# Kernel optimization log

Hardware: AMD Instinct MI355X
Metric: run time of the kernel (lower is better)

The kernel has to match this reference:

```python
import math
import jax, jax.numpy as jnp
import numpy as np

N_EXPERTS = 8
N_ACTIVE = 5
N_CAMP_A = 4
TEMPERATURE = math.e


def setup_inputs() -> dict:
    key = jax.random.key(0)
    ks = jax.random.split(key, 5)
    B, T, D, I = 4, 2048, 2048, 1024
    s = 0.02
    return {
        "x": jax.random.normal(ks[0], (B, T, D), jnp.float32),
        "Wr": jax.random.normal(ks[1], (D, N_EXPERTS), jnp.float32) * s,
        "Wg": jax.random.normal(ks[2], (N_EXPERTS, D, I), jnp.float32) * s,
        "Wu": jax.random.normal(ks[3], (N_EXPERTS, D, I), jnp.float32) * s,
        "Wd": jax.random.normal(ks[4], (N_EXPERTS, I, D), jnp.float32) * s,
    }


def _router_weights(x, Wr):
    # scores: (B,T,E)
    probs = jax.nn.softmax(jnp.einsum("btd,de->bte", x, Wr) / TEMPERATURE, axis=-1)
    _, topk_idx = jax.lax.top_k(probs, N_ACTIVE)          # (B,T,k)
    mask = jax.nn.one_hot(topk_idx, N_EXPERTS, dtype=probs.dtype).sum(axis=-2)
    w = probs * mask
    return w / (w.sum(axis=-1, keepdims=True) + 1e-8)


def reference(x, Wr, Wg, Wu, Wd):
    weights = _router_weights(x, Wr)                       # (B,T,E)
    # All experts run on full dense input (faithful to source loop), batched GEMMs.
    g = jnp.einsum("btd,edi->btei", x, Wg)                 # (B,T,E,I)
    u = jnp.einsum("btd,edi->btei", x, Wu)
    h = jax.nn.silu(g) * u
    eo = jnp.einsum("btei,eid->bted", h, Wd)               # (B,T,E,D)
    sign = jnp.concatenate([jnp.ones(N_CAMP_A), -jnp.ones(N_EXPERTS - N_CAMP_A)]).astype(x.dtype)
    output = jnp.einsum("bte,bted->btd", weights * sign, eo)  # out_a - out_g
    tension_scalar = jax.lax.stop_gradient(jnp.mean(output ** 2))
    return output, tension_scalar
```

## Files before the change

kernel.cpp:

```cpp
#include <hip/hip_runtime.h>
#include <cstdint>
#include <cstddef>


typedef short bf16x8 __attribute__((ext_vector_type(8)));
typedef float f32x4 __attribute__((ext_vector_type(4)));
typedef unsigned short u16;

typedef const unsigned int __attribute__((address_space(1)))* as1_u32p;
typedef unsigned int __attribute__((address_space(3)))* as3_u32p;

#define VMCNT6 asm volatile("s_waitcnt vmcnt(6)" ::: "memory")
#define VMCNT0 asm volatile("s_waitcnt vmcnt(0)" ::: "memory")
#define LGKM0  asm volatile("s_waitcnt lgkmcnt(0)" ::: "memory")
#define SBAR   __builtin_amdgcn_s_barrier()
#define SCHED0 __builtin_amdgcn_sched_barrier(0)
#define MFMA16(af, bf, cf) __builtin_amdgcn_mfma_f32_16x16x32_bf16(af, bf, cf, 0, 0, 0)

__device__ __forceinline__ u16 f2bf(float f) {
  unsigned u = __builtin_bit_cast(unsigned, f);
  u += 0x7fffu + ((u >> 16) & 1u);
  return (u16)(u >> 16);
}

__device__ __forceinline__ void gload16(const void* g, const u16* lds) {
  as1_u32p gp = (as1_u32p)(uintptr_t)g;
  as3_u32p lp = (as3_u32p)(unsigned)(uintptr_t)lds;
  __builtin_amdgcn_global_load_lds(gp, lp, 16, 0, 0);
}

__global__ __launch_bounds__(256) void router_kernel(
    const float* __restrict__ x, const float* __restrict__ Wr,
    float* __restrict__ Cw, u16* __restrict__ Xb) {
  const int l = threadIdx.x & 63;
  const int t = blockIdx.x * 4 + (threadIdx.x >> 6);
  const float* xr = x + (size_t)t * 2048;
  u16* xbr = Xb + (size_t)t * 2048;
  float p[8] = {0.f,0.f,0.f,0.f,0.f,0.f,0.f,0.f};
#pragma unroll
  for (int it = 0; it < 8; ++it) {
    const int d0 = it * 256 + l * 4;
    const float4 xv = *(const float4*)(xr + d0);
    unsigned lo = (unsigned)f2bf(xv.x) | ((unsigned)f2bf(xv.y) << 16);
    unsigned hi = (unsigned)f2bf(xv.z) | ((unsigned)f2bf(xv.w) << 16);
    *(unsigned*)(xbr + d0) = lo;
    *(unsigned*)(xbr + d0 + 2) = hi;
    const float xs[4] = {xv.x, xv.y, xv.z, xv.w};
#pragma unroll
    for (int jj = 0; jj < 4; ++jj) {
      const float4 w0 = *(const float4*)(Wr + (size_t)(d0 + jj) * 8);
      const float4 w1 = *(const float4*)(Wr + (size_t)(d0 + jj) * 8 + 4);
      p[0] += xs[jj] * w0.x; p[1] += xs[jj] * w0.y;
      p[2] += xs[jj] * w0.z; p[3] += xs[jj] * w0.w;
      p[4] += xs[jj] * w1.x; p[5] += xs[jj] * w1.y;
      p[6] += xs[jj] * w1.z; p[7] += xs[jj] * w1.w;
    }
  }
#pragma unroll
  for (int e = 0; e < 8; ++e) {
    float v = p[e];
#pragma unroll
    for (int off = 32; off > 0; off >>= 1) v += __shfl_xor(v, off, 64);
    p[e] = v;
  }
  constexpr float INV_TEMP = 0.36787944117144233f;
  float mx = -1e30f;
#pragma unroll
  for (int e = 0; e < 8; ++e) { p[e] *= INV_TEMP; mx = fmaxf(mx, p[e]); }
  float sum = 0.f;
#pragma unroll
  for (int e = 0; e < 8; ++e) { p[e] = __expf(p[e] - mx); sum += p[e]; }
  const float inv_sum = 1.f / sum;
#pragma unroll
  for (int e = 0; e < 8; ++e) p[e] *= inv_sum;
  unsigned sel = 0xFFu;
  for (int it = 0; it < 3; ++it) {
    float mn = 1e30f; int mi = 0;
#pragma unroll
    for (int e = 0; e < 8; ++e)
      if ((sel >> e) & 1u) { if (p[e] <= mn) { mn = p[e]; mi = e; } }
    sel &= ~(1u << mi);
  }
  float wsum = 0.f;
#pragma unroll
  for (int e = 0; e < 8; ++e) if ((sel >> e) & 1u) wsum += p[e];
  const float inv_w = 1.f / (wsum + 1e-8f);
  if (l == 0) {
#pragma unroll
    for (int e = 0; e < 8; ++e) {
      float v = ((sel >> e) & 1u) ? p[e] * inv_w : 0.f;
      Cw[(size_t)t * 8 + e] = (e < 4) ? v : -v;
    }
  }
}

__global__ __launch_bounds__(256) void tcvt_kernel(
    const float* __restrict__ in, u16* __restrict__ out,
    int R, int C, long long ZO, long long CS) {
  __shared__ float tile[32][33];
  const int z = blockIdx.z;
  const float* ib = in + (size_t)z * R * C;
  const int r0 = blockIdx.y * 32, c0 = blockIdx.x * 32;
  const int tx = threadIdx.x, ty = threadIdx.y;
#pragma unroll
  for (int j = 0; j < 4; ++j)
    tile[ty + j * 8][tx] = ib[(size_t)(r0 + ty + j * 8) * C + c0 + tx];
  __syncthreads();
#pragma unroll
  for (int j = 0; j < 4; ++j)
    out[(size_t)z * ZO + (size_t)(c0 + ty + j * 8) * CS + r0 + tx] =
        f2bf(tile[tx][ty + j * 8]);
}


__global__ __launch_bounds__(512, 2) void gemm1_8p(
    const u16* __restrict__ Xb, const u16* __restrict__ Wgt,
    const u16* __restrict__ Wut, const float* __restrict__ Cw,
    u16* __restrict__ Hp, int p) {
  extern __shared__ u16 lds[];
  const int tid = threadIdx.x;
  const int l = tid & 63, w = tid >> 6;
  const int wr = w >> 2, wc = w & 3;
  const int lq = l >> 4, lr = l & 15;
  const int bid = blockIdx.x;
  const int work = (bid & 7) * 128 + (bid >> 3);
  const int mtile = work & 31;
  const int en = work >> 5;
  const int el = en >> 3, nt = en & 7;
  const int e = p * 4 + el;
  const u16* gA  = Xb + (size_t)mtile * 256 * 2048;
  const u16* s0p = Wgt + (size_t)e * 2097152 + (size_t)nt * 128 * 2048;
  const u16* s1p = Wut + (size_t)e * 2097152 + (size_t)nt * 128 * 2048;
  const u16* s2p = gA;
  const u16* s3p = gA + (size_t)128 * 2048;
  const int NT = 32;

  auto stageU = [&](int tt, const u16* srcb, int u) {
    if (tt >= NT) return;
    u16* dst = lds + (tt & 1) * 32768 + u * 8192;
    const int kt = tt * 64;
#pragma unroll
    for (int j = 0; j < 2; ++j) {
      const int g = j * 512 + tid;
      const int row = g >> 3;
      const int cg = (g & 7) ^ (row & 7);
      gload16(srcb + (size_t)row * 2048 + kt + cg * 8, dst + g * 8);
    }
  };

  const int xr = lr & 7;
  const int x0 = (lq ^ xr) * 8;
  const int x1 = ((4 + lq) ^ xr) * 8;
  const int aB = (2 + wr) * 8192 + lr * 64;
  const int gBo = (wc * 32 + lr) * 64;
  const int uBo = 8192 + (wc * 32 + lr) * 64;

  bf16x8 a[8][2], bg[2][2], bu[2][2];
  f32x4 ag[8][2], au[8][2];
#pragma unroll
  for (int mi = 0; mi < 8; ++mi)
#pragma unroll
    for (int ni = 0; ni < 2; ++ni) {
      ag[mi][ni] = (f32x4){0.f, 0.f, 0.f, 0.f};
      au[mi][ni] = (f32x4){0.f, 0.f, 0.f, 0.f};
    }

  stageU(0, s0p, 0); stageU(0, s1p, 1); stageU(0, s2p, 2); stageU(0, s3p, 3);
  stageU(1, s0p, 0); stageU(1, s1p, 1); stageU(1, s2p, 2);
  VMCNT6; SBAR;

  for (int t = 0; t < NT; ++t) {
    const u16* Lb = lds + (t & 1) * 32768;
    {
#pragma unroll
      for (int mi = 0; mi < 4; ++mi) {
        a[mi][0] = *(const bf16x8*)&Lb[aB + mi * 1024 + x0];
        a[mi][1] = *(const bf16x8*)&Lb[aB + mi * 1024 + x1];
      }
#pragma unroll
      for (int ni = 0; ni < 2; ++ni) {
        bg[ni][0] = *(const bf16x8*)&Lb[gBo + ni * 1024 + x0];
        bg[ni][1] = *(const bf16x8*)&Lb[gBo + ni * 1024 + x1];
      }
      stageU(t + 1, s3p, 3);
      SBAR; LGKM0; SCHED0;
      __builtin_amdgcn_s_setprio(1);
#pragma unroll
      for (int mi = 0; mi < 4; ++mi)
#pragma unroll
        for (int ni = 0; ni < 2; ++ni)
#pragma unroll
          for (int kk = 0; kk < 2; ++kk)
            ag[mi][ni] = MFMA16(a[mi][kk], bg[ni][kk], ag[mi][ni]);
      __builtin_amdgcn_s_setprio(0); SCHED0; SBAR;
    }
    {
#pragma unroll
      for (int ni = 0; ni < 2; ++ni) {
        bu[ni][0] = *(const bf16x8*)&Lb[uBo + ni * 1024 + x0];
        bu[ni][1] = *(const bf16x8*)&Lb[uBo + ni * 1024 + x1];
      }
      stageU(t + 2, s0p, 0);
      SBAR; LGKM0; SCHED0;
      __builtin_amdgcn_s_setprio(1);
#pragma unroll
      for (int mi = 0; mi < 4; ++mi)
#pragma unroll
        for (int ni = 0; ni < 2; ++ni)
#pragma unroll
          for (int kk = 0; kk < 2; ++kk)
            au[mi][ni] = MFMA16(a[mi][kk], bu[ni][kk], au[mi][ni]);
      __builtin_amdgcn_s_setprio(0); SCHED0; SBAR;
    }
    {
#pragma unroll
      for (int mi = 4; mi < 8; ++mi) {
        a[mi][0] = *(const bf16x8*)&Lb[aB + mi * 1024 + x0];
        a[mi][1] = *(const bf16x8*)&Lb[aB + mi * 1024 + x1];
      }
      stageU(t + 2, s1p, 1);
      SBAR; LGKM0; SCHED0;
      __builtin_amdgcn_s_setprio(1);
#pragma unroll
      for (int mi = 4; mi < 8; ++mi)
#pragma unroll
        for (int ni = 0; ni < 2; ++ni)
#pragma unroll
          for (int kk = 0; kk < 2; ++kk)
            ag[mi][ni] = MFMA16(a[mi][kk], bg[ni][kk], ag[mi][ni]);
      __builtin_amdgcn_s_setprio(0); SCHED0; SBAR;
    }
    {
      stageU(t + 2, s2p, 2);
      if (t < NT - 2) { VMCNT6; } else if (t == NT - 2) { VMCNT0; }
      SBAR; LGKM0; SCHED0;
      __builtin_amdgcn_s_setprio(1);
#pragma unroll
      for (int mi = 4; mi < 8; ++mi)
#pragma unroll
        for (int ni = 0; ni < 2; ++ni)
#pragma unroll
          for (int kk = 0; kk < 2; ++kk)
            au[mi][ni] = MFMA16(a[mi][kk], bu[ni][kk], au[mi][ni]);
      __builtin_amdgcn_s_setprio(0); SCHED0; SBAR;
    }
  }

  __syncthreads();
  float* cl = (float*)lds;
  if (tid < 256) cl[tid] = Cw[(size_t)(mtile * 256 + tid) * 8 + e];
  __syncthreads();
#pragma unroll
  for (int mi = 0; mi < 8; ++mi) {
#pragma unroll
    for (int j = 0; j < 4; ++j) {
      const int rl = wr * 128 + mi * 16 + lq * 4 + j;
      const float c = cl[rl];
      const size_t row = (size_t)mtile * 256 + rl;
#pragma unroll
      for (int ni = 0; ni < 2; ++ni) {
        const float g = ag[mi][ni][j], u = au[mi][ni][j];
        const float h = g * (1.f / (1.f + __expf(-g))) * u * c;
        Hp[row * 4096 + el * 1024 + nt * 128 + wc * 32 + ni * 16 + lr] = f2bf(h);
      }
    }
  }
}

__global__ __launch_bounds__(512, 2) void gemm2_8p(
    const u16* __restrict__ Hp, const u16* __restrict__ Wdt,
    float* __restrict__ out, int koff, int accum) {
  extern __shared__ u16 lds[];
  const int tid = threadIdx.x;
  const int l = tid & 63, w = tid >> 6;
  const int wr = w >> 2, wc = w & 3;
  const int lq = l >> 4, lr = l & 15;
  const int bid = blockIdx.x;
  const int work = (bid & 7) * 32 + (bid >> 3);
  const int mtile = work & 31, ntile = work >> 5;
  const u16* gA = Hp + (size_t)mtile * 256 * 4096;
  const u16* gB = Wdt + (size_t)ntile * 256 * 8192 + koff;
  const u16* s0p = gB;
  const u16* s1p = gB + (size_t)128 * 8192;
  const u16* s2p = gA;
  const u16* s3p = gA + (size_t)128 * 4096;
  const int NT = 64;

  auto stageU = [&](int tt, const u16* srcb, int stride, int u) {
    if (tt >= NT) return;
    u16* dst = lds + (tt & 1) * 32768 + u * 8192;
    const int kt = tt * 64;
#pragma unroll
    for (int j = 0; j < 2; ++j) {
      const int g = j * 512 + tid;
      const int row = g >> 3;
      const int cg = (g & 7) ^ (row & 7);
      gload16(srcb + (size_t)row * stride + kt + cg * 8, dst + g * 8);
    }
  };

  const int xr = lr & 7;
  const int x0 = (lq ^ xr) * 8;
  const int x1 = ((4 + lq) ^ xr) * 8;
  const int aB = (2 + wr) * 8192 + lr * 64;
  const int bB = (wc >> 1) * 8192 + ((wc & 1) * 64 + lr) * 64;

  bf16x8 a[8][2], b[4][2];
  f32x4 acc[8][4];
#pragma unroll
  for (int mi = 0; mi < 8; ++mi)
#pragma unroll
    for (int ni = 0; ni < 4; ++ni) acc[mi][ni] = (f32x4){0.f, 0.f, 0.f, 0.f};

  stageU(0, s0p, 8192, 0); stageU(0, s1p, 8192, 1);
  stageU(0, s2p, 4096, 2); stageU(0, s3p, 4096, 3);
  stageU(1, s0p, 8192, 0); stageU(1, s1p, 8192, 1); stageU(1, s2p, 4096, 2);
  VMCNT6; SBAR;

  for (int t = 0; t < NT; ++t) {
    const u16* Lb = lds + (t & 1) * 32768;
    {
#pragma unroll
      for (int mi = 0; mi < 4; ++mi) {
        a[mi][0] = *(const bf16x8*)&Lb[aB + mi * 1024 + x0];
        a[mi][1] = *(const bf16x8*)&Lb[aB + mi * 1024 + x1];
      }
#pragma unroll
      for (int ni = 0; ni < 2; ++ni) {
        b[ni][0] = *(const bf16x8*)&Lb[bB + ni * 1024 + x0];
        b[ni][1] = *(const bf16x8*)&Lb[bB + ni * 1024 + x1];
      }
      if (wc < 2) {
#pragma unroll
        for (int ni = 2; ni < 4; ++ni) {
          b[ni][0] = *(const bf16x8*)&Lb[bB + ni * 1024 + x0];
          b[ni][1] = *(const bf16x8*)&Lb[bB + ni * 1024 + x1];
        }
      }
      stageU(t + 1, s3p, 4096, 3);
      SBAR; LGKM0; SCHED0;
      __builtin_amdgcn_s_setprio(1);
#pragma unroll
      for (int mi = 0; mi < 4; ++mi)
#pragma unroll
        for (int ni = 0; ni < 2; ++ni)
#pragma unroll
          for (int kk = 0; kk < 2; ++kk)
            acc[mi][ni] = MFMA16(a[mi][kk], b[ni][kk], acc[mi][ni]);
      __builtin_amdgcn_s_setprio(0); SCHED0; SBAR;
    }
    {
      if (wc >= 2) {
#pragma unroll
        for (int ni = 2; ni < 4; ++ni) {
          b[ni][0] = *(const bf16x8*)&Lb[bB + ni * 1024 + x0];
          b[ni][1] = *(const bf16x8*)&Lb[bB + ni * 1024 + x1];
        }
      }
      stageU(t + 2, s0p, 8192, 0);
      SBAR; LGKM0; SCHED0;
      __builtin_amdgcn_s_setprio(1);
#pragma unroll
      for (int mi = 0; mi < 4; ++mi)
#pragma unroll
        for (int ni = 2; ni < 4; ++ni)
#pragma unroll
          for (int kk = 0; kk < 2; ++kk)
            acc[mi][ni] = MFMA16(a[mi][kk], b[ni][kk], acc[mi][ni]);
      __builtin_amdgcn_s_setprio(0); SCHED0; SBAR;
    }
    {
#pragma unroll
      for (int mi = 4; mi < 8; ++mi) {
        a[mi][0] = *(const bf16x8*)&Lb[aB + mi * 1024 + x0];
        a[mi][1] = *(const bf16x8*)&Lb[aB + mi * 1024 + x1];
      }
      stageU(t + 2, s1p, 8192, 1);
      SBAR; LGKM0; SCHED0;
      __builtin_amdgcn_s_setprio(1);
#pragma unroll
      for (int mi = 4; mi < 8; ++mi)
#pragma unroll
        for (int ni = 2; ni < 4; ++ni)
#pragma unroll
          for (int kk = 0; kk < 2; ++kk)
            acc[mi][ni] = MFMA16(a[mi][kk], b[ni][kk], acc[mi][ni]);
      __builtin_amdgcn_s_setprio(0); SCHED0; SBAR;
    }
    {
      stageU(t + 2, s2p, 4096, 2);
      if (t < NT - 2) { VMCNT6; } else if (t == NT - 2) { VMCNT0; }
      SBAR; LGKM0; SCHED0;
      __builtin_amdgcn_s_setprio(1);
#pragma unroll
      for (int mi = 4; mi < 8; ++mi)
#pragma unroll
        for (int ni = 0; ni < 2; ++ni)
#pragma unroll
          for (int kk = 0; kk < 2; ++kk)
            acc[mi][ni] = MFMA16(a[mi][kk], b[ni][kk], acc[mi][ni]);
      __builtin_amdgcn_s_setprio(0); SCHED0; SBAR;
    }
  }

#pragma unroll
  for (int mi = 0; mi < 8; ++mi)
#pragma unroll
    for (int ni = 0; ni < 4; ++ni)
#pragma unroll
      for (int j = 0; j < 4; ++j) {
        const int row = mtile * 256 + wr * 128 + mi * 16 + lq * 4 + j;
        const int col = ntile * 256 + wc * 64 + ni * 16 + lr;
        const size_t idx = (size_t)row * 2048 + col;
        float v = acc[mi][ni][j];
        if (accum) v += out[idx];
        out[idx] = v;
      }
}

__global__ __launch_bounds__(256) void sqsum_partial(
    const float* __restrict__ out, float* __restrict__ part, int n4) {
  float s = 0.f;
  const int idx = blockIdx.x * 256 + threadIdx.x;
  const int stride = gridDim.x * 256;
  for (int i = idx; i < n4; i += stride) {
    const float4 v = ((const float4*)out)[i];
    s += v.x * v.x + v.y * v.y + v.z * v.z + v.w * v.w;
  }
#pragma unroll
  for (int off = 32; off > 0; off >>= 1) s += __shfl_down(s, off, 64);
  __shared__ float ls[4];
  if ((threadIdx.x & 63) == 0) ls[threadIdx.x >> 6] = s;
  __syncthreads();
  if (threadIdx.x == 0) part[blockIdx.x] = ls[0] + ls[1] + ls[2] + ls[3];
}

__global__ __launch_bounds__(256) void sqsum_final(
    const float* __restrict__ part, float* __restrict__ dst, int np, float scale) {
  float s = 0.f;
  for (int i = threadIdx.x; i < np; i += 256) s += part[i];
#pragma unroll
  for (int off = 32; off > 0; off >>= 1) s += __shfl_down(s, off, 64);
  __shared__ float ls[4];
  if ((threadIdx.x & 63) == 0) ls[threadIdx.x >> 6] = s;
  __syncthreads();
  if (threadIdx.x == 0) dst[0] = (ls[0] + ls[1] + ls[2] + ls[3]) * scale;
}

extern "C" void kernel_launch(void* const* d_in, const int* in_sizes, int n_in,
                              void* d_out, int out_size, void* d_ws, size_t ws_size,
                              hipStream_t stream) {
  (void)in_sizes; (void)n_in; (void)out_size; (void)ws_size;
  const float* x  = (const float*)d_in[0];
  const float* Wr = (const float*)d_in[1];
  const float* Wg = (const float*)d_in[2];
  const float* Wu = (const float*)d_in[3];
  const float* Wd = (const float*)d_in[4];
  float* out = (float*)d_out;
  char* ws = (char*)d_ws;
  u16*   Xb   = (u16*)(ws);
  u16*   Wgt  = (u16*)(ws + 33554432);
  u16*   Wut  = (u16*)(ws + 67108864);
  u16*   Wdt  = (u16*)(ws + 100663296);
  u16*   Hp   = (u16*)(ws + 134217728);
  float* Cw   = (float*)(ws + 201326592);
  float* part = (float*)(ws + 201588736);

  (void)hipFuncSetAttribute((const void*)gemm1_8p,
                            hipFuncAttributeMaxDynamicSharedMemorySize, 131072);
  (void)hipFuncSetAttribute((const void*)gemm2_8p,
                            hipFuncAttributeMaxDynamicSharedMemorySize, 131072);

  router_kernel<<<2048, 256, 0, stream>>>(x, Wr, Cw, Xb);

  dim3 tb(32, 8);
  tcvt_kernel<<<dim3(32, 64, 8), tb, 0, stream>>>(Wg, Wgt, 2048, 1024, 2097152LL, 2048LL);
  tcvt_kernel<<<dim3(32, 64, 8), tb, 0, stream>>>(Wu, Wut, 2048, 1024, 2097152LL, 2048LL);
  tcvt_kernel<<<dim3(64, 32, 8), tb, 0, stream>>>(Wd, Wdt, 1024, 2048, 1024LL, 8192LL);

  for (int p = 0; p < 2; ++p) {
    gemm1_8p<<<1024, 512, 131072, stream>>>(Xb, Wgt, Wut, Cw, Hp, p);
    gemm2_8p<<<256, 512, 131072, stream>>>(Hp, Wdt, out, p * 4096, p);
  }

  sqsum_partial<<<1024, 256, 0, stream>>>(out, part, 16777216 / 4);
  sqsum_final<<<1, 256, 0, stream>>>(part, out + 16777216, 1024, 1.f / 16777216.f);
}
```

Measured before the change: 884.6 us.

## Make gemm1 persistent over four N-tiles per block and transpose router weights

gemm1 now launches 256 blocks instead of 1024. Each block loops over four (expert, N-tile) work items while keeping the same X row tile, and the weight-tile prefetch runs continuously across item boundaries. The epilogue reads the combine weights from a transposed expert-major array with float4 loads, which removes the LDS staging and syncthreads. Load addressing is precomputed and an extra partial lgkmcnt wait is added before the barrier. The intent is to cut launch and tail overhead and pipeline bubbles between tiles, at the cost of fewer, longer blocks that may balance worse across CUs.

```diff
diff --git a/kernel.cpp b/kernel.cpp
--- a/kernel.cpp
+++ b/kernel.cpp
@@ -13,6 +13,7 @@
 #define VMCNT6 asm volatile("s_waitcnt vmcnt(6)" ::: "memory")
 #define VMCNT0 asm volatile("s_waitcnt vmcnt(0)" ::: "memory")
 #define LGKM0  asm volatile("s_waitcnt lgkmcnt(0)" ::: "memory")
+#define LGKM8  asm volatile("s_waitcnt lgkmcnt(8)" ::: "memory")
 #define SBAR   __builtin_amdgcn_s_barrier()
 #define SCHED0 __builtin_amdgcn_sched_barrier(0)
 #define MFMA16(af, bf, cf) __builtin_amdgcn_mfma_f32_16x16x32_bf16(af, bf, cf, 0, 0, 0)
@@ -31,7 +32,7 @@
 
 __global__ __launch_bounds__(256) void router_kernel(
     const float* __restrict__ x, const float* __restrict__ Wr,
-    float* __restrict__ Cw, u16* __restrict__ Xb) {
+    float* __restrict__ CwT, u16* __restrict__ Xb) {
   const int l = threadIdx.x & 63;
   const int t = blockIdx.x * 4 + (threadIdx.x >> 6);
   const float* xr = x + (size_t)t * 2048;
@@ -89,7 +90,7 @@
 #pragma unroll
     for (int e = 0; e < 8; ++e) {
       float v = ((sel >> e) & 1u) ? p[e] * inv_w : 0.f;
-      Cw[(size_t)t * 8 + e] = (e < 4) ? v : -v;
+      CwT[(size_t)e * 8192 + t] = (e < 4) ? v : -v;
     }
   }
 }
@@ -115,37 +116,40 @@
 
 __global__ __launch_bounds__(512, 2) void gemm1_8p(
     const u16* __restrict__ Xb, const u16* __restrict__ Wgt,
-    const u16* __restrict__ Wut, const float* __restrict__ Cw,
+    const u16* __restrict__ Wut, const float* __restrict__ CwT,
     u16* __restrict__ Hp, int p) {
   extern __shared__ u16 lds[];
   const int tid = threadIdx.x;
   const int l = tid & 63, w = tid >> 6;
   const int wr = w >> 2, wc = w & 3;
   const int lq = l >> 4, lr = l & 15;
-  const int bid = blockIdx.x;
-  const int work = (bid & 7) * 128 + (bid >> 3);
-  const int mtile = work & 31;
-  const int en = work >> 5;
-  const int el = en >> 3, nt = en & 7;
-  const int e = p * 4 + el;
+  const int b = blockIdx.x;
+  const int xcd = b & 7;
+  const int mtile = b >> 3;
+  const int en0 = xcd * 4;
   const u16* gA  = Xb + (size_t)mtile * 256 * 2048;
-  const u16* s0p = Wgt + (size_t)e * 2097152 + (size_t)nt * 128 * 2048;
-  const u16* s1p = Wut + (size_t)e * 2097152 + (size_t)nt * 128 * 2048;
   const u16* s2p = gA;
   const u16* s3p = gA + (size_t)128 * 2048;
-  const int NT = 32;
-
-  auto stageU = [&](int tt, const u16* srcb, int u) {
-    if (tt >= NT) return;
-    u16* dst = lds + (tt & 1) * 32768 + u * 8192;
-    const int kt = tt * 64;
-#pragma unroll
-    for (int j = 0; j < 2; ++j) {
-      const int g = j * 512 + tid;
-      const int row = g >> 3;
-      const int cg = (g & 7) ^ (row & 7);
-      gload16(srcb + (size_t)row * 2048 + kt + cg * 8, dst + g * 8);
-    }
+
+  const int row0 = tid >> 3,          cg0 = (tid & 7) ^ (row0 & 7);
+  const int row1 = (512 + tid) >> 3,  cg1 = ((512 + tid) & 7) ^ (row1 & 7);
+  const int off0 = row0 * 2048 + cg0 * 8;
+  const int off1 = row1 * 2048 + cg1 * 8;
+  const int d0e = tid * 8, d1e = (512 + tid) * 8;
+
+  auto bptr = [&](const u16* base, int item) -> const u16* {
+    const int it = item > 3 ? 3 : item;
+    const int en = en0 + it;
+    return base + (size_t)(p * 4 + (en >> 3)) * 2097152 +
+           (size_t)(en & 7) * 128 * 2048;
+  };
+
+  auto stageV = [&](int vt2, const u16* srcb, int u) {
+    if (vt2 >= 128) return;
+    u16* dst = lds + (vt2 & 1) * 32768 + u * 8192;
+    const int kt = (vt2 & 31) * 64;
+    gload16(srcb + (size_t)(off0 + kt), dst + d0e);
+    gload16(srcb + (size_t)(off1 + kt), dst + d1e);
   };
 
   const int xr = lr & 7;
@@ -165,12 +169,18 @@
       au[mi][ni] = (f32x4){0.f, 0.f, 0.f, 0.f};
     }
 
-  stageU(0, s0p, 0); stageU(0, s1p, 1); stageU(0, s2p, 2); stageU(0, s3p, 3);
-  stageU(1, s0p, 0); stageU(1, s1p, 1); stageU(1, s2p, 2);
+  const u16* bgS = bptr(Wgt, 0);
+  const u16* buS = bptr(Wut, 0);
+  int item_c = 0;
+
+  stageV(0, bgS, 0); stageV(0, buS, 1); stageV(0, s2p, 2); stageV(0, s3p, 3);
+  stageV(1, bgS, 0); stageV(1, buS, 1); stageV(1, s2p, 2);
   VMCNT6; SBAR;
 
-  for (int t = 0; t < NT; ++t) {
-    const u16* Lb = lds + (t & 1) * 32768;
+  for (int vt = 0; vt < 128; ++vt) {
+    const int t = vt & 31;
+    if (t == 30) { bgS = bptr(Wgt, item_c + 1); buS = bptr(Wut, item_c + 1); }
+    const u16* Lb = lds + (vt & 1) * 32768;
     {
 #pragma unroll
       for (int mi = 0; mi < 4; ++mi) {
@@ -182,8 +192,8 @@
         bg[ni][0] = *(const bf16x8*)&Lb[gBo + ni * 1024 + x0];
         bg[ni][1] = *(const bf16x8*)&Lb[gBo + ni * 1024 + x1];
       }
-      stageU(t + 1, s3p, 3);
-      SBAR; LGKM0; SCHED0;
+      stageV(vt + 1, s3p, 3);
+      LGKM8; SBAR; LGKM0; SCHED0;
       __builtin_amdgcn_s_setprio(1);
 #pragma unroll
       for (int mi = 0; mi < 4; ++mi)
@@ -200,7 +210,7 @@
         bu[ni][0] = *(const bf16x8*)&Lb[uBo + ni * 1024 + x0];
         bu[ni][1] = *(const bf16x8*)&Lb[uBo + ni * 1024 + x1];
       }
-      stageU(t + 2, s0p, 0);
+      stageV(vt + 2, bgS, 0);
       SBAR; LGKM0; SCHED0;
       __builtin_amdgcn_s_setprio(1);
 #pragma unroll
@@ -218,7 +228,7 @@
         a[mi][0] = *(const bf16x8*)&Lb[aB + mi * 1024 + x0];
         a[mi][1] = *(const bf16x8*)&Lb[aB + mi * 1024 + x1];
       }
-      stageU(t + 2, s1p, 1);
+      stageV(vt + 2, buS, 1);
       SBAR; LGKM0; SCHED0;
       __builtin_amdgcn_s_setprio(1);
 #pragma unroll
@@ -231,8 +241,8 @@
       __builtin_amdgcn_s_setprio(0); SCHED0; SBAR;
     }
     {
-      stageU(t + 2, s2p, 2);
-      if (t < NT - 2) { VMCNT6; } else if (t == NT - 2) { VMCNT0; }
+      stageV(vt + 2, s2p, 2);
+      if (vt < 126) { VMCNT6; } else if (vt == 126) { VMCNT0; }
       SBAR; LGKM0; SCHED0;
       __builtin_amdgcn_s_setprio(1);
 #pragma unroll
@@ -244,25 +254,35 @@
             au[mi][ni] = MFMA16(a[mi][kk], bu[ni][kk], au[mi][ni]);
       __builtin_amdgcn_s_setprio(0); SCHED0; SBAR;
     }
-  }
-
-  __syncthreads();
-  float* cl = (float*)lds;
-  if (tid < 256) cl[tid] = Cw[(size_t)(mtile * 256 + tid) * 8 + e];
-  __syncthreads();
-#pragma unroll
-  for (int mi = 0; mi < 8; ++mi) {
-#pragma unroll
-    for (int j = 0; j < 4; ++j) {
-      const int rl = wr * 128 + mi * 16 + lq * 4 + j;
-      const float c = cl[rl];
-      const size_t row = (size_t)mtile * 256 + rl;
-#pragma unroll
-      for (int ni = 0; ni < 2; ++ni) {
-        const float g = ag[mi][ni][j], u = au[mi][ni][j];
-        const float h = g * (1.f / (1.f + __expf(-g))) * u * c;
-        Hp[row * 4096 + el * 1024 + nt * 128 + wc * 32 + ni * 16 + lr] = f2bf(h);
-      }
+    if (t == 31) {
+      const int en = en0 + item_c;
+      const int el = en >> 3, nt = en & 7, e = p * 4 + el;
+      const float* cb = CwT + (size_t)e * 8192 + mtile * 256;
+#pragma unroll
+      for (int mi = 0; mi < 8; ++mi) {
+        const int r0 = wr * 128 + mi * 16 + lq * 4;
+        const float4 c4 = *(const float4*)(cb + r0);
+        const float cs[4] = {c4.x, c4.y, c4.z, c4.w};
+#pragma unroll
+        for (int j = 0; j < 4; ++j) {
+          const size_t row = (size_t)mtile * 256 + r0 + j;
+#pragma unroll
+          for (int ni = 0; ni < 2; ++ni) {
+            const float g = ag[mi][ni][j], u = au[mi][ni][j];
+            const float h = g * (1.f / (1.f + __expf(-g))) * u * cs[j];
+            Hp[row * 4096 + el * 1024 + nt * 128 + wc * 32 + ni * 16 + lr] =
+                f2bf(h);
+          }
+        }
+      }
+      ++item_c;
+#pragma unroll
+      for (int mi = 0; mi < 8; ++mi)
+#pragma unroll
+        for (int ni = 0; ni < 2; ++ni) {
+          ag[mi][ni] = (f32x4){0.f, 0.f, 0.f, 0.f};
+          au[mi][ni] = (f32x4){0.f, 0.f, 0.f, 0.f};
+        }
     }
   }
 }
@@ -286,17 +306,25 @@
   const u16* s3p = gA + (size_t)128 * 4096;
   const int NT = 64;
 
-  auto stageU = [&](int tt, const u16* srcb, int stride, int u) {
+  const int row0 = tid >> 3,          cg0 = (tid & 7) ^ (row0 & 7);
+  const int row1 = (512 + tid) >> 3,  cg1 = ((512 + tid) & 7) ^ (row1 & 7);
+  const int offA0 = row0 * 4096 + cg0 * 8, offA1 = row1 * 4096 + cg1 * 8;
+  const int offB0 = row0 * 8192 + cg0 * 8, offB1 = row1 * 8192 + cg1 * 8;
+  const int d0e = tid * 8, d1e = (512 + tid) * 8;
+
+  auto stageA = [&](int tt, const u16* srcb, int u) {
     if (tt >= NT) return;
     u16* dst = lds + (tt & 1) * 32768 + u * 8192;
     const int kt = tt * 64;
-#pragma unroll
-    for (int j = 0; j < 2; ++j) {
-      const int g = j * 512 + tid;
-      const int row = g >> 3;
-      const int cg = (g & 7) ^ (row & 7);
-      gload16(srcb + (size_t)row * stride + kt + cg * 8, dst + g * 8);
-    }
+    gload16(srcb + (size_t)(offA0 + kt), dst + d0e);
+    gload16(srcb + (size_t)(offA1 + kt), dst + d1e);
+  };
+  auto stageB = [&](int tt, const u16* srcb, int u) {
+    if (tt >= NT) return;
+    u16* dst = lds + (tt & 1) * 32768 + u * 8192;
+    const int kt = tt * 64;
+    gload16(srcb + (size_t)(offB0 + kt), dst + d0e);
+    gload16(srcb + (size_t)(offB1 + kt), dst + d1e);
   };
 
   const int xr = lr & 7;
@@ -312,9 +340,8 @@
 #pragma unroll
     for (int ni = 0; ni < 4; ++ni) acc[mi][ni] = (f32x4){0.f, 0.f, 0.f, 0.f};
 
-  stageU(0, s0p, 8192, 0); stageU(0, s1p, 8192, 1);
-  stageU(0, s2p, 4096, 2); stageU(0, s3p, 4096, 3);
-  stageU(1, s0p, 8192, 0); stageU(1, s1p, 8192, 1); stageU(1, s2p, 4096, 2);
+  stageB(0, s0p, 0); stageB(0, s1p, 1); stageA(0, s2p, 2); stageA(0, s3p, 3);
+  stageB(1, s0p, 0); stageB(1, s1p, 1); stageA(1, s2p, 2);
   VMCNT6; SBAR;
 
   for (int t = 0; t < NT; ++t) {
@@ -337,8 +364,8 @@
           b[ni][1] = *(const bf16x8*)&Lb[bB + ni * 1024 + x1];
         }
       }
-      stageU(t + 1, s3p, 4096, 3);
-      SBAR; LGKM0; SCHED0;
+      stageA(t + 1, s3p, 3);
+      LGKM8; SBAR; LGKM0; SCHED0;
       __builtin_amdgcn_s_setprio(1);
 #pragma unroll
       for (int mi = 0; mi < 4; ++mi)
@@ -357,7 +384,7 @@
           b[ni][1] = *(const bf16x8*)&Lb[bB + ni * 1024 + x1];
         }
       }
-      stageU(t + 2, s0p, 8192, 0);
+      stageB(t + 2, s0p, 0);
       SBAR; LGKM0; SCHED0;
       __builtin_amdgcn_s_setprio(1);
 #pragma unroll
@@ -375,7 +402,7 @@
         a[mi][0] = *(const bf16x8*)&Lb[aB + mi * 1024 + x0];
         a[mi][1] = *(const bf16x8*)&Lb[aB + mi * 1024 + x1];
       }
-      stageU(t + 2, s1p, 8192, 1);
+      stageB(t + 2, s1p, 1);
       SBAR; LGKM0; SCHED0;
       __builtin_amdgcn_s_setprio(1);
 #pragma unroll
@@ -388,7 +415,7 @@
       __builtin_amdgcn_s_setprio(0); SCHED0; SBAR;
     }
     {
-      stageU(t + 2, s2p, 4096, 2);
+      stageA(t + 2, s2p, 2);
       if (t < NT - 2) { VMCNT6; } else if (t == NT - 2) { VMCNT0; }
       SBAR; LGKM0; SCHED0;
       __builtin_amdgcn_s_setprio(1);
@@ -463,7 +490,7 @@
   u16*   Wut  = (u16*)(ws + 67108864);
   u16*   Wdt  = (u16*)(ws + 100663296);
   u16*   Hp   = (u16*)(ws + 134217728);
-  float* Cw   = (float*)(ws + 201326592);
+  float* CwT  = (float*)(ws + 201326592);
   float* part = (float*)(ws + 201588736);
 
   (void)hipFuncSetAttribute((const void*)gemm1_8p,
@@ -471,7 +498,7 @@
   (void)hipFuncSetAttribute((const void*)gemm2_8p,
                             hipFuncAttributeMaxDynamicSharedMemorySize, 131072);
 
-  router_kernel<<<2048, 256, 0, stream>>>(x, Wr, Cw, Xb);
+  router_kernel<<<2048, 256, 0, stream>>>(x, Wr, CwT, Xb);
 
   dim3 tb(32, 8);
   tcvt_kernel<<<dim3(32, 64, 8), tb, 0, stream>>>(Wg, Wgt, 2048, 1024, 2097152LL, 2048LL);
@@ -479,7 +506,7 @@
   tcvt_kernel<<<dim3(64, 32, 8), tb, 0, stream>>>(Wd, Wdt, 1024, 2048, 1024LL, 8192LL);
 
   for (int p = 0; p < 2; ++p) {
-    gemm1_8p<<<1024, 512, 131072, stream>>>(Xb, Wgt, Wut, Cw, Hp, p);
+    gemm1_8p<<<256, 512, 131072, stream>>>(Xb, Wgt, Wut, CwT, Hp, p);
     gemm2_8p<<<256, 512, 131072, stream>>>(Hp, Wdt, out, p * 4096, p);
   }
 
```

New measurement: 903.3 us. +2.1%, slower.

## Restructure down-projection GEMM pipeline to prefetch LDS fragments across phases

Applied to the files above, without the earlier changes.

The gemm2 main loop is unrolled by two with explicit ping-pong buffers. Each phase now uses a single k-slice for all four B columns, with partial lgkmcnt waits, and the next tile's B and first A fragments are read from LDS during the last MFMA phase. Staging addresses are precomputed once per thread. In the gate/up kernel the per-tile routing coefficients are read straight from global memory instead of through an LDS staging step with two syncthreads. The risks are higher register pressure from the extra fragment arrays and subtle wait-count correctness.

```diff
diff --git a/kernel.cpp b/kernel.cpp
--- a/kernel.cpp
+++ b/kernel.cpp
@@ -13,8 +13,12 @@
 #define VMCNT6 asm volatile("s_waitcnt vmcnt(6)" ::: "memory")
 #define VMCNT0 asm volatile("s_waitcnt vmcnt(0)" ::: "memory")
 #define LGKM0  asm volatile("s_waitcnt lgkmcnt(0)" ::: "memory")
+#define LGKM4  asm volatile("s_waitcnt lgkmcnt(4)" ::: "memory")
+#define LGKM8  asm volatile("s_waitcnt lgkmcnt(8)" ::: "memory")
 #define SBAR   __builtin_amdgcn_s_barrier()
 #define SCHED0 __builtin_amdgcn_sched_barrier(0)
+#define PRIO1  __builtin_amdgcn_s_setprio(1)
+#define PRIO0  __builtin_amdgcn_s_setprio(0)
 #define MFMA16(af, bf, cf) __builtin_amdgcn_mfma_f32_16x16x32_bf16(af, bf, cf, 0, 0, 0)
 
 __device__ __forceinline__ u16 f2bf(float f) {
@@ -184,7 +188,7 @@
       }
       stageU(t + 1, s3p, 3);
       SBAR; LGKM0; SCHED0;
-      __builtin_amdgcn_s_setprio(1);
+      PRIO1;
 #pragma unroll
       for (int mi = 0; mi < 4; ++mi)
 #pragma unroll
@@ -192,7 +196,7 @@
 #pragma unroll
           for (int kk = 0; kk < 2; ++kk)
             ag[mi][ni] = MFMA16(a[mi][kk], bg[ni][kk], ag[mi][ni]);
-      __builtin_amdgcn_s_setprio(0); SCHED0; SBAR;
+      PRIO0; SCHED0; SBAR;
     }
     {
 #pragma unroll
@@ -202,7 +206,7 @@
       }
       stageU(t + 2, s0p, 0);
       SBAR; LGKM0; SCHED0;
-      __builtin_amdgcn_s_setprio(1);
+      PRIO1;
 #pragma unroll
       for (int mi = 0; mi < 4; ++mi)
 #pragma unroll
@@ -210,7 +214,7 @@
 #pragma unroll
           for (int kk = 0; kk < 2; ++kk)
             au[mi][ni] = MFMA16(a[mi][kk], bu[ni][kk], au[mi][ni]);
-      __builtin_amdgcn_s_setprio(0); SCHED0; SBAR;
+      PRIO0; SCHED0; SBAR;
     }
     {
 #pragma unroll
@@ -220,7 +224,7 @@
       }
       stageU(t + 2, s1p, 1);
       SBAR; LGKM0; SCHED0;
-      __builtin_amdgcn_s_setprio(1);
+      PRIO1;
 #pragma unroll
       for (int mi = 4; mi < 8; ++mi)
 #pragma unroll
@@ -228,13 +232,13 @@
 #pragma unroll
           for (int kk = 0; kk < 2; ++kk)
             ag[mi][ni] = MFMA16(a[mi][kk], bg[ni][kk], ag[mi][ni]);
-      __builtin_amdgcn_s_setprio(0); SCHED0; SBAR;
+      PRIO0; SCHED0; SBAR;
     }
     {
       stageU(t + 2, s2p, 2);
       if (t < NT - 2) { VMCNT6; } else if (t == NT - 2) { VMCNT0; }
       SBAR; LGKM0; SCHED0;
-      __builtin_amdgcn_s_setprio(1);
+      PRIO1;
 #pragma unroll
       for (int mi = 4; mi < 8; ++mi)
 #pragma unroll
@@ -242,26 +246,22 @@
 #pragma unroll
           for (int kk = 0; kk < 2; ++kk)
             au[mi][ni] = MFMA16(a[mi][kk], bu[ni][kk], au[mi][ni]);
-      __builtin_amdgcn_s_setprio(0); SCHED0; SBAR;
-    }
-  }
-
-  __syncthreads();
-  float* cl = (float*)lds;
-  if (tid < 256) cl[tid] = Cw[(size_t)(mtile * 256 + tid) * 8 + e];
-  __syncthreads();
+      PRIO0; SCHED0; SBAR;
+    }
+  }
+
 #pragma unroll
   for (int mi = 0; mi < 8; ++mi) {
 #pragma unroll
     for (int j = 0; j < 4; ++j) {
-      const int rl = wr * 128 + mi * 16 + lq * 4 + j;
-      const float c = cl[rl];
-      const size_t row = (size_t)mtile * 256 + rl;
+      const int row = mtile * 256 + wr * 128 + mi * 16 + lq * 4 + j;
+      const float c = Cw[(size_t)row * 8 + e];
 #pragma unroll
       for (int ni = 0; ni < 2; ++ni) {
         const float g = ag[mi][ni][j], u = au[mi][ni][j];
         const float h = g * (1.f / (1.f + __expf(-g))) * u * c;
-        Hp[row * 4096 + el * 1024 + nt * 128 + wc * 32 + ni * 16 + lr] = f2bf(h);
+        Hp[(size_t)row * 4096 + el * 1024 + nt * 128 + wc * 32 + ni * 16 + lr] =
+            f2bf(h);
       }
     }
   }
@@ -286,17 +286,25 @@
   const u16* s3p = gA + (size_t)128 * 4096;
   const int NT = 64;
 
-  auto stageU = [&](int tt, const u16* srcb, int stride, int u) {
+  const int row0 = tid >> 3,          cg0 = (tid & 7) ^ (row0 & 7);
+  const int row1 = (512 + tid) >> 3,  cg1 = ((512 + tid) & 7) ^ (row1 & 7);
+  const int offA0 = row0 * 4096 + cg0 * 8, offA1 = row1 * 4096 + cg1 * 8;
+  const int offB0 = row0 * 8192 + cg0 * 8, offB1 = row1 * 8192 + cg1 * 8;
+  const int d0e = tid * 8, d1e = (512 + tid) * 8;
+
+  auto stageA = [&](int tt, const u16* srcb, int u) {
     if (tt >= NT) return;
     u16* dst = lds + (tt & 1) * 32768 + u * 8192;
     const int kt = tt * 64;
-#pragma unroll
-    for (int j = 0; j < 2; ++j) {
-      const int g = j * 512 + tid;
-      const int row = g >> 3;
-      const int cg = (g & 7) ^ (row & 7);
-      gload16(srcb + (size_t)row * stride + kt + cg * 8, dst + g * 8);
-    }
+    gload16(srcb + (size_t)(offA0 + kt), dst + d0e);
+    gload16(srcb + (size_t)(offA1 + kt), dst + d1e);
+  };
+  auto stageB = [&](int tt, const u16* srcb, int u) {
+    if (tt >= NT) return;
+    u16* dst = lds + (tt & 1) * 32768 + u * 8192;
+    const int kt = tt * 64;
+    gload16(srcb + (size_t)(offB0 + kt), dst + d0e);
+    gload16(srcb + (size_t)(offB1 + kt), dst + d1e);
   };
 
   const int xr = lr & 7;
@@ -305,101 +313,151 @@
   const int aB = (2 + wr) * 8192 + lr * 64;
   const int bB = (wc >> 1) * 8192 + ((wc & 1) * 64 + lr) * 64;
 
-  bf16x8 a[8][2], b[4][2];
+  bf16x8 a03k0[4], a03k1[4], a47k0[4], a47k1[4];
+  bf16x8 bk0[4], bk1A[4], bk1B[4];
   f32x4 acc[8][4];
 #pragma unroll
   for (int mi = 0; mi < 8; ++mi)
 #pragma unroll
     for (int ni = 0; ni < 4; ++ni) acc[mi][ni] = (f32x4){0.f, 0.f, 0.f, 0.f};
 
-  stageU(0, s0p, 8192, 0); stageU(0, s1p, 8192, 1);
-  stageU(0, s2p, 4096, 2); stageU(0, s3p, 4096, 3);
-  stageU(1, s0p, 8192, 0); stageU(1, s1p, 8192, 1); stageU(1, s2p, 4096, 2);
+  stageB(0, s0p, 0); stageB(0, s1p, 1); stageA(0, s2p, 2); stageA(0, s3p, 3);
+  stageB(1, s0p, 0); stageB(1, s1p, 1); stageA(1, s2p, 2);
   VMCNT6; SBAR;
-
-  for (int t = 0; t < NT; ++t) {
-    const u16* Lb = lds + (t & 1) * 32768;
+  {
+    const u16* Lb = lds;
+#pragma unroll
+    for (int ni = 0; ni < 4; ++ni) bk0[ni]  = *(const bf16x8*)&Lb[bB + ni * 1024 + x0];
+#pragma unroll
+    for (int ni = 0; ni < 4; ++ni) bk1A[ni] = *(const bf16x8*)&Lb[bB + ni * 1024 + x1];
+#pragma unroll
+    for (int mi = 0; mi < 4; ++mi) a03k0[mi] = *(const bf16x8*)&Lb[aB + mi * 1024 + x0];
+  }
+
+  for (int i = 0; i < NT / 2; ++i) {
     {
-#pragma unroll
-      for (int mi = 0; mi < 4; ++mi) {
-        a[mi][0] = *(const bf16x8*)&Lb[aB + mi * 1024 + x0];
-        a[mi][1] = *(const bf16x8*)&Lb[aB + mi * 1024 + x1];
-      }
-#pragma unroll
-      for (int ni = 0; ni < 2; ++ni) {
-        b[ni][0] = *(const bf16x8*)&Lb[bB + ni * 1024 + x0];
-        b[ni][1] = *(const bf16x8*)&Lb[bB + ni * 1024 + x1];
-      }
-      if (wc < 2) {
-#pragma unroll
-        for (int ni = 2; ni < 4; ++ni) {
-          b[ni][0] = *(const bf16x8*)&Lb[bB + ni * 1024 + x0];
-          b[ni][1] = *(const bf16x8*)&Lb[bB + ni * 1024 + x1];
-        }
-      }
-      stageU(t + 1, s3p, 4096, 3);
+      const int t = 2 * i;
+      const u16* Lb  = lds;
+      const u16* Lbn = lds + 32768;
+#pragma unroll
+      for (int mi = 0; mi < 4; ++mi)
+        a03k1[mi] = *(const bf16x8*)&Lb[aB + mi * 1024 + x1];
+      stageA(t + 1, s3p, 3);
+      SBAR; LGKM4; SCHED0;
+      PRIO1;
+#pragma unroll
+      for (int mi = 0; mi < 4; ++mi)
+#pragma unroll
+        for (int ni = 0; ni < 4; ++ni)
+          acc[mi][ni] = MFMA16(a03k0[mi], bk0[ni], acc[mi][ni]);
+      PRIO0; SCHED0; SBAR;
+#pragma unroll
+      for (int mi = 0; mi < 4; ++mi)
+        a47k0[mi] = *(const bf16x8*)&Lb[aB + (4 + mi) * 1024 + x0];
+#pragma unroll
+      for (int mi = 0; mi < 4; ++mi)
+        a47k1[mi] = *(const bf16x8*)&Lb[aB + (4 + mi) * 1024 + x1];
+      stageB(t + 2, s0p, 0);
+      SBAR; LGKM8; SCHED0;
+      PRIO1;
+#pragma unroll
+      for (int mi = 0; mi < 4; ++mi)
+#pragma unroll
+        for (int ni = 0; ni < 4; ++ni)
+          acc[mi][ni] = MFMA16(a03k1[mi], bk1A[ni], acc[mi][ni]);
+      PRIO0; SCHED0; SBAR;
+      stageB(t + 2, s1p, 1);
       SBAR; LGKM0; SCHED0;
-      __builtin_amdgcn_s_setprio(1);
-#pragma unroll
-      for (int mi = 0; mi < 4; ++mi)
-#pragma unroll
-        for (int ni = 0; ni < 2; ++ni)
-#pragma unroll
-          for (int kk = 0; kk < 2; ++kk)
-            acc[mi][ni] = MFMA16(a[mi][kk], b[ni][kk], acc[mi][ni]);
-      __builtin_amdgcn_s_setprio(0); SCHED0; SBAR;
+      PRIO1;
+#pragma unroll
+      for (int mi = 0; mi < 4; ++mi)
+#pragma unroll
+        for (int ni = 0; ni < 4; ++ni)
+          acc[4 + mi][ni] = MFMA16(a47k0[mi], bk0[ni], acc[4 + mi][ni]);
+      PRIO0; SCHED0; SBAR;
+      stageA(t + 2, s2p, 2);
+      if (t < NT - 2) { VMCNT6; } else { VMCNT0; }
+      SBAR;
+#pragma unroll
+      for (int ni = 0; ni < 4; ++ni)
+        bk0[ni]  = *(const bf16x8*)&Lbn[bB + ni * 1024 + x0];
+#pragma unroll
+      for (int ni = 0; ni < 4; ++ni)
+        bk1B[ni] = *(const bf16x8*)&Lbn[bB + ni * 1024 + x1];
+#pragma unroll
+      for (int mi = 0; mi < 4; ++mi)
+        a03k0[mi] = *(const bf16x8*)&Lbn[aB + mi * 1024 + x0];
+      SCHED0;
+      PRIO1;
+#pragma unroll
+      for (int mi = 0; mi < 4; ++mi)
+#pragma unroll
+        for (int ni = 0; ni < 4; ++ni)
+          acc[4 + mi][ni] = MFMA16(a47k1[mi], bk1A[ni], acc[4 + mi][ni]);
+      PRIO0; SCHED0; SBAR;
     }
     {
-      if (wc >= 2) {
-#pragma unroll
-        for (int ni = 2; ni < 4; ++ni) {
-          b[ni][0] = *(const bf16x8*)&Lb[bB + ni * 1024 + x0];
-          b[ni][1] = *(const bf16x8*)&Lb[bB + ni * 1024 + x1];
-        }
-      }
-      stageU(t + 2, s0p, 8192, 0);
+      const int t = 2 * i + 1;
+      const u16* Lb  = lds + 32768;
+      const u16* Lbn = lds;
+#pragma unroll
+      for (int mi = 0; mi < 4; ++mi)
+        a03k1[mi] = *(const bf16x8*)&Lb[aB + mi * 1024 + x1];
+      stageA(t + 1, s3p, 3);
+      SBAR; LGKM4; SCHED0;
+      PRIO1;
+#pragma unroll
+      for (int mi = 0; mi < 4; ++mi)
+#pragma unroll
+        for (int ni = 0; ni < 4; ++ni)
+          acc[mi][ni] = MFMA16(a03k0[mi], bk0[ni], acc[mi][ni]);
+      PRIO0; SCHED0; SBAR;
+#pragma unroll
+      for (int mi = 0; mi < 4; ++mi)
+        a47k0[mi] = *(const bf16x8*)&Lb[aB + (4 + mi) * 1024 + x0];
+#pragma unroll
+      for (int mi = 0; mi < 4; ++mi)
+        a47k1[mi] = *(const bf16x8*)&Lb[aB + (4 + mi) * 1024 + x1];
+      stageB(t + 2, s0p, 0);
+      SBAR; LGKM8; SCHED0;
+      PRIO1;
+#pragma unroll
+      for (int mi = 0; mi < 4; ++mi)
+#pragma unroll
+        for (int ni = 0; ni < 4; ++ni)
+          acc[mi][ni] = MFMA16(a03k1[mi], bk1B[ni], acc[mi][ni]);
+      PRIO0; SCHED0; SBAR;
+      stageB(t + 2, s1p, 1);
       SBAR; LGKM0; SCHED0;
-      __builtin_amdgcn_s_setprio(1);
-#pragma unroll
-      for (int mi = 0; mi < 4; ++mi)
-#pragma unroll
-        for (int ni = 2; ni < 4; ++ni)
-#pragma unroll
-          for (int kk = 0; kk < 2; ++kk)
-            acc[mi][ni] = MFMA16(a[mi][kk], b[ni][kk], acc[mi][ni]);
-      __builtin_amdgcn_s_setprio(0); SCHED0; SBAR;
-    }
-    {
-#pragma unroll
-      for (int mi = 4; mi < 8; ++mi) {
-        a[mi][0] = *(const bf16x8*)&Lb[aB + mi * 1024 + x0];
-        a[mi][1] = *(const bf16x8*)&Lb[aB + mi * 1024 + x1];
-      }
-      stageU(t + 2, s1p, 8192, 1);
-      SBAR; LGKM0; SCHED0;
-      __builtin_amdgcn_s_setprio(1);
-#pragma unroll
-      for (int mi = 4; mi < 8; ++mi)
-#pragma unroll
-        for (int ni = 2; ni < 4; ++ni)
-#pragma unroll
-          for (int kk = 0; kk < 2; ++kk)
-            acc[mi][ni] = MFMA16(a[mi][kk], b[ni][kk], acc[mi][ni]);
-      __builtin_amdgcn_s_setprio(0); SCHED0; SBAR;
-    }
-    {
-      stageU(t + 2, s2p, 4096, 2);
-      if (t < NT - 2) { VMCNT6; } else if (t == NT - 2) { VMCNT0; }
-      SBAR; LGKM0; SCHED0;
-      __builtin_amdgcn_s_setprio(1);
-#pragma unroll
-      for (int mi = 4; mi < 8; ++mi)
-#pragma unroll
-        for (int ni = 0; ni < 2; ++ni)
-#pragma unroll
-          for (int kk = 0; kk < 2; ++kk)
-            acc[mi][ni] = MFMA16(a[mi][kk], b[ni][kk], acc[mi][ni]);
-      __builtin_amdgcn_s_setprio(0); SCHED0; SBAR;
+      PRIO1;
+#pragma unroll
+      for (int mi = 0; mi < 4; ++mi)
+#pragma unroll
+        for (int ni = 0; ni < 4; ++ni)
+          acc[4 + mi][ni] = MFMA16(a47k0[mi], bk0[ni], acc[4 + mi][ni]);
+      PRIO0; SCHED0; SBAR;
+      stageA(t + 2, s2p, 2);
+      if (t < NT - 2) { VMCNT6; }
+      SBAR;
+      if (i < NT / 2 - 1) {
+#pragma unroll
+        for (int ni = 0; ni < 4; ++ni)
+          bk0[ni]  = *(const bf16x8*)&Lbn[bB + ni * 1024 + x0];
+#pragma unroll
+        for (int ni = 0; ni < 4; ++ni)
+          bk1A[ni] = *(const bf16x8*)&Lbn[bB + ni * 1024 + x1];
+#pragma unroll
+        for (int mi = 0; mi < 4; ++mi)
+          a03k0[mi] = *(const bf16x8*)&Lbn[aB + mi * 1024 + x0];
+      }
+      SCHED0;
+      PRIO1;
+#pragma unroll
+      for (int mi = 0; mi < 4; ++mi)
+#pragma unroll
+        for (int ni = 0; ni < 4; ++ni)
+          acc[4 + mi][ni] = MFMA16(a47k1[mi], bk1B[ni], acc[4 + mi][ni]);
+      PRIO0; SCHED0; SBAR;
     }
   }
 
```

New measurement: 955.8 us. +8.1%, slower.
